# Optimization experiments

Measured on AMD Instinct MI355X. Metric: run time of the kernel, lower is better.

Reference implementation:

```python
import jax, jax.numpy as jnp
import numpy as np
from jax import lax

B, K, S = 1, 4, 1024
D = 1024          # hidden_size
DI = 2048         # intermediate_size = 2*D (expand=2)
N = 16            # ssm state size
DT_RANK = 64      # ceil(D/16)
CONV_K = 4
N_LAYERS = 48
CARD = 2048       # vocab
EPS = 1e-5


def setup_inputs() -> dict:
    key = jax.random.key(0)
    ks = jax.random.split(key, 10)
    sc = 0.02
    sequence = jax.random.randint(ks[0], (B, K, S), 0, CARD)
    emb_W = jax.random.normal(ks[1], (K, CARD, D), jnp.float32) * sc
    norm_w = jnp.ones((N_LAYERS, D), jnp.float32)
    in_W = jax.random.normal(ks[2], (N_LAYERS, 2 * DI, D), jnp.float32) * sc
    conv_w = jax.random.normal(ks[3], (N_LAYERS, DI, CONV_K), jnp.float32) * sc
    conv_b = jnp.zeros((N_LAYERS, DI), jnp.float32)
    x_W = jax.random.normal(ks[4], (N_LAYERS, DT_RANK + 2 * N, DI), jnp.float32) * sc
    dt_W = jax.random.normal(ks[5], (N_LAYERS, DI, DT_RANK), jnp.float32) * sc
    dt_b = jax.random.normal(ks[6], (N_LAYERS, DI), jnp.float32) * 0.1
    # HF Mamba init: A_log = log([1..N]) broadcast over channels
    A_log = jnp.log(jnp.broadcast_to(jnp.arange(1, N + 1, dtype=jnp.float32), (N_LAYERS, DI, N)))
    D_skip = jnp.ones((N_LAYERS, DI), jnp.float32)
    out_W = jax.random.normal(ks[7], (N_LAYERS, D, DI), jnp.float32) * sc
    normf_w = jnp.ones((D,), jnp.float32)
    head_W = jax.random.normal(ks[8], (K, CARD, D), jnp.float32) * sc
    head_b = jnp.zeros((K, CARD), jnp.float32)
    return {"sequence": sequence, "emb_W": emb_W, "norm_w": norm_w, "in_W": in_W,
            "conv_w": conv_w, "conv_b": conv_b, "x_W": x_W, "dt_W": dt_W, "dt_b": dt_b,
            "A_log": A_log, "D_skip": D_skip, "out_W": out_W, "normf_w": normf_w,
            "head_W": head_W, "head_b": head_b}


def rmsnorm(x, w):
    return x * lax.rsqrt(jnp.mean(x * x, -1, keepdims=True) + EPS) * w


def mamba_block(x, p):
    """One HF MambaBlock: residual + RMSNorm + MambaMixer (selective scan)."""
    norm_w, in_W, conv_w, conv_b, x_W, dt_W, dt_b, A_log, D_skip, out_W = p
    res = x
    h = rmsnorm(x, norm_w)
    proj = h @ in_W.T                                  # (B,S,2*DI)
    xz, gate = jnp.split(proj, 2, axis=-1)
    # causal depthwise conv1d, kernel 4
    xc = jnp.transpose(xz, (0, 2, 1))                  # (B,DI,S)
    xc = lax.conv_general_dilated(xc, conv_w[:, None, :], (1,), [(CONV_K - 1, 0)],
                                  feature_group_count=DI,
                                  dimension_numbers=("NCH", "OIH", "NCH"))
    xc = xc + conv_b[None, :, None]
    u = jax.nn.silu(jnp.transpose(xc, (0, 2, 1)))      # (B,S,DI)
    ssm_in = u @ x_W.T                                 # (B,S,DT_RANK+2N)
    dt_r, Bm, Cm = jnp.split(ssm_in, [DT_RANK, DT_RANK + N], axis=-1)
    dt = jax.nn.softplus(dt_r @ dt_W.T + dt_b)         # (B,S,DI)
    A = -jnp.exp(A_log)                                # (DI,N)

    def step(hst, inp):
        dt_t, B_t, C_t, u_t = inp                      # (B,DI),(B,N),(B,N),(B,DI)
        dA = jnp.exp(dt_t[:, :, None] * A)             # (B,DI,N)
        hst = dA * hst + (dt_t * u_t)[:, :, None] * B_t[:, None, :]
        y = jnp.einsum("bdn,bn->bd", hst, C_t)
        return hst, y

    h0 = jnp.zeros((B, DI, N), x.dtype)
    _, ys = lax.scan(step, h0, (dt.swapaxes(0, 1), Bm.swapaxes(0, 1),
                                Cm.swapaxes(0, 1), u.swapaxes(0, 1)))
    y = ys.swapaxes(0, 1) + u * D_skip                 # (B,S,DI)
    y = y * jax.nn.silu(gate)
    return res + y @ out_W.T


mamba_block_ckpt = jax.checkpoint(mamba_block)


def reference(sequence, emb_W, norm_w, in_W, conv_w, conv_b, x_W, dt_W, dt_b,
              A_log, D_skip, out_W, normf_w, head_W, head_b):
    # sum of K token-stream embeddings
    x = emb_W[jnp.arange(K)[None, :, None], sequence].sum(1)   # (B,S,D)

    def layer(x, p):
        return mamba_block_ckpt(x, p), None

    x, _ = lax.scan(layer, x, (norm_w, in_W, conv_w, conv_b, x_W, dt_W, dt_b,
                               A_log, D_skip, out_W))
    x = rmsnorm(x, normf_w)
    logits = jnp.einsum("bsd,kvd->bksv", x, head_W) + head_b[None, :, None, :]
    return logits                                              # (B,K,S,CARD)
```

## Files before the change

### kernel.cpp

```cpp
#include <hip/hip_runtime.h>
#include <hip/hip_bf16.h>

#define S 1024
#define D 1024
#define DI 2048
#define NSTATE 16
#define DTR 64
#define XPD 96
#define NL 48
#define CARD 2048
#define KTOK 4

typedef __attribute__((ext_vector_type(8))) short bf16x8;
typedef __attribute__((ext_vector_type(4))) float f32x4;
struct __align__(16) US8 { unsigned long long a, b; };

__device__ __forceinline__ unsigned short f2bf(float f) {
    unsigned u = __builtin_bit_cast(unsigned, f);
    return (unsigned short)((u + 0x7fffu + ((u >> 16) & 1u)) >> 16);
}
__device__ __forceinline__ float bf2f(unsigned short u) {
    return __builtin_bit_cast(float, (unsigned)u << 16);
}
__device__ __forceinline__ float fsilu(float x) { return x / (1.f + __expf(-x)); }
__device__ __forceinline__ float fsoftplus(float x) {
    return fmaxf(x, 0.f) + log1pf(__expf(-fabsf(x)));
}
template<int CTRL>
__device__ __forceinline__ float dpp_add(float v) {
    int m = __builtin_amdgcn_update_dpp(0, __builtin_bit_cast(int, v), CTRL, 0xF, 0xF, true);
    return v + __builtin_bit_cast(float, m);
}
__device__ __forceinline__ void gload_lds16(const void* g, void* l) {
    __builtin_amdgcn_global_load_lds((const __attribute__((address_space(1))) void*)g,
                                     (__attribute__((address_space(3))) void*)l, 16, 0, 0);
}
template<int N> __device__ __forceinline__ void wait_vm() {
    if constexpr (N == 0)      asm volatile("s_waitcnt vmcnt(0)" ::: "memory");
    else if constexpr (N == 3) asm volatile("s_waitcnt vmcnt(3)" ::: "memory");
    else if constexpr (N == 4) asm volatile("s_waitcnt vmcnt(4)" ::: "memory");
    else if constexpr (N == 6) asm volatile("s_waitcnt vmcnt(6)" ::: "memory");
    else                       asm volatile("s_waitcnt vmcnt(8)" ::: "memory");
}

__global__ __launch_bounds__(256) void cvt4_kernel(const float* __restrict__ a, long NA,
                                                   const float* __restrict__ b, long NB,
                                                   const float* __restrict__ c, long NC,
                                                   const float* __restrict__ d, long ND,
                                                   unsigned short* __restrict__ oa,
                                                   unsigned short* __restrict__ ob,
                                                   unsigned short* __restrict__ oc,
                                                   unsigned short* __restrict__ od) {
    long i = (long)blockIdx.x * 256 + threadIdx.x;
    const float* src; unsigned short* dst; long off;
    if (i < NA)                    { src = a; dst = oa; off = i; }
    else if (i < NA + NB)          { src = b; dst = ob; off = i - NA; }
    else if (i < NA + NB + NC)     { src = c; dst = oc; off = i - NA - NB; }
    else                            { src = d; dst = od; off = i - NA - NB - NC; }
    f32x4 v0 = *(const f32x4*)&src[off * 8];
    f32x4 v1 = *(const f32x4*)&src[off * 8 + 4];
    US8 pk;
    pk.a = (unsigned long long)f2bf(v0[0]) | ((unsigned long long)f2bf(v0[1]) << 16)
         | ((unsigned long long)f2bf(v0[2]) << 32) | ((unsigned long long)f2bf(v0[3]) << 48);
    pk.b = (unsigned long long)f2bf(v1[0]) | ((unsigned long long)f2bf(v1[1]) << 16)
         | ((unsigned long long)f2bf(v1[2]) << 32) | ((unsigned long long)f2bf(v1[3]) << 48);
    *(US8*)&dst[off * 8] = pk;
}

__global__ __launch_bounds__(256) void embed_kernel(const int* __restrict__ seq,
                                                    const float* __restrict__ embW,
                                                    float* __restrict__ x) {
    int s = blockIdx.x, t = threadIdx.x;
    f32x4 acc = (f32x4)0.f;
#pragma unroll
    for (int k = 0; k < KTOK; ++k) {
        int tok = seq[k * S + s];
        const f32x4 v = *(const f32x4*)&embW[((size_t)k * CARD + tok) * D + t * 4];
        acc += v;
    }
    *(f32x4*)&x[(size_t)s * D + t * 4] = acc;
}

__global__ __launch_bounds__(256) void rmsnorm_kernel(const float* __restrict__ x,
                                                      const float* __restrict__ w,
                                                      unsigned short* __restrict__ o) {
    int row = blockIdx.x, t = threadIdx.x;
    f32x4 v = *(const f32x4*)&x[(size_t)row * D + t * 4];
    float ss = v[0]*v[0] + v[1]*v[1] + v[2]*v[2] + v[3]*v[3];
#pragma unroll
    for (int off = 32; off >= 1; off >>= 1) ss += __shfl_xor(ss, off);
    __shared__ float red[4];
    int wave = t >> 6, lane = t & 63;
    if (lane == 0) red[wave] = ss;
    __syncthreads();
    ss = red[0] + red[1] + red[2] + red[3];
    float rs = rsqrtf(ss * (1.f / D) + 1e-5f);
    f32x4 wv = *(const f32x4*)&w[t * 4];
    unsigned long long pk = 0;
#pragma unroll
    for (int j = 0; j < 4; ++j)
        pk |= (unsigned long long)f2bf(v[j] * rs * wv[j]) << (16 * j);
    *(unsigned long long*)&o[(size_t)row * D + t * 4] = pk;
}

__global__ __launch_bounds__(256) void outred_rms_kernel(const float* __restrict__ part,
                                                         float* __restrict__ x,
                                                         const float* __restrict__ w,
                                                         unsigned short* __restrict__ o) {
    int row = blockIdx.x, t = threadIdx.x;
    size_t base = (size_t)row * D + t * 4;
    f32x4 v = *(const f32x4*)&x[base];
#pragma unroll
    for (int j = 0; j < 2; ++j)
        v += *(const f32x4*)&part[(size_t)j * (S * D) + base];
    *(f32x4*)&x[base] = v;
    float ss = v[0]*v[0] + v[1]*v[1] + v[2]*v[2] + v[3]*v[3];
#pragma unroll
    for (int off = 32; off >= 1; off >>= 1) ss += __shfl_xor(ss, off);
    __shared__ float red[4];
    int wave = t >> 6, lane = t & 63;
    if (lane == 0) red[wave] = ss;
    __syncthreads();
    ss = red[0] + red[1] + red[2] + red[3];
    float rs = rsqrtf(ss * (1.f / D) + 1e-5f);
    f32x4 wv = *(const f32x4*)&w[t * 4];
    unsigned long long pk = 0;
#pragma unroll
    for (int j = 0; j < 4; ++j)
        pk |= (unsigned long long)f2bf(v[j] * rs * wv[j]) << (16 * j);
    *(unsigned long long*)&o[base] = pk;
}

__global__ __launch_bounds__(256) void ssm_reduce_kernel(const float* __restrict__ part,
                                                         float* __restrict__ ssm,
                                                         unsigned short* __restrict__ ssmb) {
    int i = blockIdx.x * 256 + threadIdx.x;
    float a = 0.f;
#pragma unroll
    for (int j = 0; j < 8; ++j)
        a += part[(size_t)j * (S * XPD) + i];
    ssm[i] = a;
    ssmb[i] = f2bf(a);
}

__global__ __launch_bounds__(256) void conv_silu_kernel(const float* __restrict__ proj,
                                                        const float* __restrict__ cw,
                                                        const float* __restrict__ cb,
                                                        unsigned short* __restrict__ ub) {
    int idx = blockIdx.x * 256 + threadIdx.x;
    int s = idx >> 11, c = idx & (DI - 1);
    f32x4 w = *(const f32x4*)&cw[c * 4];
    float acc = cb[c];
#pragma unroll
    for (int t = 0; t < 4; ++t) {
        int ss = s - 3 + t;
        if (ss >= 0) acc = fmaf(w[t], proj[(size_t)ss * 4096 + c], acc);
    }
    ub[idx] = f2bf(acc * (1.f / (1.f + __expf(-acc))));
}

__global__ __launch_bounds__(1024, 2) void scan2_kernel(const unsigned short* __restrict__ ssmb,
                                                        const unsigned short* __restrict__ dtWb,
                                                        const float* __restrict__ dtb,
                                                        const unsigned short* __restrict__ ub,
                                                        const float* __restrict__ ssm,
                                                        const float* __restrict__ proj,
                                                        const float* __restrict__ A_log,
                                                        const float* __restrict__ Dsk,
                                                        unsigned short* __restrict__ yfb) {
    __shared__ float sdu[S * 4 * 2];
    __shared__ float sP[1024], sQ[1024];

    const int tid = threadIdx.x;
    const int d0 = blockIdx.x * 4;
    const int chunk = tid >> 6;
    const int lane = tid & 63;
    const int dl = (tid >> 4) & 3;
    const int n = tid & 15;
    const int sbase = chunk * 64;

#pragma unroll
    for (int i = 0; i < 4; ++i) {
        int idx = tid + i * 1024;
        int s = idx >> 2, d2 = idx & 3;
        sdu[idx * 2 + 1] = bf2f(ub[(size_t)s * DI + d0 + d2]);
    }

    {
        const int lr = lane & 15;
        const int lk = (lane >> 4) << 3;
        f32x4 dacc[4];
#pragma unroll
        for (int m = 0; m < 4; ++m) dacc[m] = (f32x4)0.f;
        bf16x8 wf0 = *(const bf16x8*)&dtWb[(size_t)(d0 + lr) * DTR + lk];
        bf16x8 wf1 = *(const bf16x8*)&dtWb[(size_t)(d0 + lr) * DTR + 32 + lk];
#pragma unroll
        for (int m = 0; m < 4; ++m) {
            const unsigned short* arow = &ssmb[(size_t)(sbase + m * 16 + lr) * XPD];
            bf16x8 a0 = *(const bf16x8*)&arow[lk];
            bf16x8 a1 = *(const bf16x8*)&arow[32 + lk];
            dacc[m] = __builtin_amdgcn_mfma_f32_16x16x32_bf16(a0, wf0, dacc[m], 0, 0, 0);
            dacc[m] = __builtin_amdgcn_mfma_f32_16x16x32_bf16(a1, wf1, dacc[m], 0, 0, 0);
        }
        if (lr < 4) {
            float bias = dtb[d0 + lr];
            const int rb = (lane >> 4) << 2;
#pragma unroll
            for (int m = 0; m < 4; ++m)
#pragma unroll
                for (int j = 0; j < 4; ++j) {
                    int sl = sbase + m * 16 + rb + j;
                    sdu[(sl * 4 + lr) * 2 + 0] = fsoftplus(dacc[m][j] + bias);
                }
        }
    }
    const float Av = -__expf(A_log[(d0 + dl) * NSTATE + n]);
    const float Dv = Dsk[d0 + dl];
    __syncthreads();

    float h = 0.f, P = 1.f;
#pragma unroll 4
    for (int i = 0; i < 64; ++i) {
        int s = sbase + i;
        float2 du = *(const float2*)&sdu[(s * 4 + dl) * 2];
        float Bs  = ssm[s * XPD + DTR + n];
        float dA  = __expf(du.x * Av);
        P *= dA;
        h = fmaf(dA, h, du.x * du.y * Bs);
    }
    const int pqb = (dl * 16 + n) * 16;
    sP[pqb + chunk] = P;
    sQ[pqb + chunk] = h;
    __syncthreads();
    float hi = 0.f;
    for (int j = 0; j < chunk; ++j) hi = fmaf(sP[pqb + j], hi, sQ[pqb + j]);
    h = hi;
#pragma unroll 2
    for (int i = 0; i < 64; ++i) {
        int s = sbase + i;
        float2 du = *(const float2*)&sdu[(s * 4 + dl) * 2];
        float Bs  = ssm[s * XPD + DTR + n];
        float Cs  = ssm[s * XPD + DTR + NSTATE + n];
        float dA  = __expf(du.x * Av);
        h = fmaf(dA, h, du.x * du.y * Bs);
        float pc = h * Cs;
        pc = dpp_add<0xB1>(pc);
        pc = dpp_add<0x4E>(pc);
        pc = dpp_add<0x124>(pc);
        pc = dpp_add<0x128>(pc);
        if (n == 0) {
            float g = proj[(size_t)s * 4096 + 2048 + d0 + dl];
            yfb[(size_t)s * DI + d0 + dl] = f2bf((pc + du.y * Dv) * fsilu(g));
        }
    }
}

template<int MR, int NR, int EPI, int KSPLIT, int ABF16, int DBUF>
__global__ __launch_bounds__(256) void gemm_bt(const void* __restrict__ Av, int lda,
                                               const unsigned short* __restrict__ W,
                                               float* __restrict__ C,
                                               int K, int N,
                                               const float* __restrict__ bias) {
    constexpr int BM = MR * 32;
    constexpr int BN = NR * 32;
    static_assert(DBUF == 0 || ((BM == 64 || BM == 128) && BN == 128 && ABF16 == 1), "dbuf shape");
    constexpr int NBUF = DBUF ? 3 : 1;
    __shared__ unsigned short As[NBUF][BM][32];
    __shared__ unsigned short Ws[NBUF][BN][32];
    const int tid = threadIdx.x;
    const int lane = tid & 63;
    const int wave = tid >> 6;
    const int wr = wave >> 1, wc = wave & 1;
    const int m0 = blockIdx.y * BM;
    const int n0 = blockIdx.x * BN;
    const unsigned short* Wp = W;
    const float* biasp = bias;
    float* Cp = C;
    if (EPI == 3) {
        size_t z = blockIdx.z;
        Wp += z * (size_t)N * K;
        Cp += z * (size_t)1024 * N;
        biasp += z * N;
    }
    if (EPI == 5)
        Cp = C + (size_t)blockIdx.z * 1024 * N;
    f32x4 acc[MR][NR];
#pragma unroll
    for (int m = 0; m < MR; ++m)
#pragma unroll
        for (int n = 0; n < NR; ++n) acc[m][n] = (f32x4)0.f;

    const int lr = lane & 15;
    const int lk = (lane >> 4) << 3;
    const int grow = lane >> 2;
    const int gcol = (lane & 3) << 3;

    const int kc = (KSPLIT > 1) ? blockIdx.z : 0;
    const int Kc = K / KSPLIT;
    const int kbeg = kc * Kc;

    if constexpr (DBUF) {
        const unsigned short* Ab = (const unsigned short*)Av;
        const int nt = Kc >> 5;
        constexpr int L = BM / 64 + 2;
        auto ISSUE = [&](int t, int buf) {
            const int k0 = kbeg + t * 32;
#pragma unroll
            for (int u2 = wave; u2 < BM / 16; u2 += 4)
                gload_lds16(&Ab[(size_t)(m0 + u2 * 16 + grow) * lda + k0 + gcol],
                            &As[buf][u2 * 16][0]);
#pragma unroll
            for (int u2 = wave; u2 < BN / 16; u2 += 4)
                gload_lds16(&Wp[(size_t)(n0 + u2 * 16 + grow) * K + k0 + gcol],
                            &Ws[buf][u2 * 16][0]);
        };
        ISSUE(0, 0);
        if (nt > 1) ISSUE(1, 1);
        int nb = 2;
        int cb = 0;
        for (int t = 0; t < nt; ++t) {
            if (t + 2 < nt) {
                ISSUE(t + 2, nb);
                if (++nb == 3) nb = 0;
            }
            const int rem = nt - 1 - t;
            if (rem >= 2)      wait_vm<2 * L>();
            else if (rem == 1) wait_vm<L>();
            else               wait_vm<0>();
            __builtin_amdgcn_s_barrier();
            bf16x8 af[MR], wf[NR];
#pragma unroll
            for (int m = 0; m < MR; ++m)
                af[m] = *(const bf16x8*)&As[cb][wr * (MR * 16) + m * 16 + lr][lk];
#pragma unroll
            for (int n = 0; n < NR; ++n)
                wf[n] = *(const bf16x8*)&Ws[cb][wc * (NR * 16) + n * 16 + lr][lk];
            asm volatile("s_waitcnt lgkmcnt(0)" ::: "memory");
            __builtin_amdgcn_s_barrier();
            if (++cb == 3) cb = 0;
#pragma unroll
            for (int m = 0; m < MR; ++m)
#pragma unroll
                for (int n = 0; n < NR; ++n)
                    acc[m][n] = __builtin_amdgcn_mfma_f32_16x16x32_bf16(af[m], wf[n], acc[m][n], 0, 0, 0);
        }
    } else {
        for (int k0 = kbeg; k0 < kbeg + Kc; k0 += 32) {
            __syncthreads();
            if (ABF16) {
                const unsigned short* Ab = (const unsigned short*)Av;
#pragma unroll
                for (int u2 = wave; u2 < BM / 16; u2 += 4)
                    gload_lds16(&Ab[(size_t)(m0 + u2 * 16 + grow) * lda + k0 + gcol],
                                &As[0][u2 * 16][0]);
            } else {
                const float* Af = (const float*)Av;
#pragma unroll
                for (int i = 0; i < BM / 32; ++i) {
                    int idx = tid + i * 256;
                    int row = idx >> 3, c4 = (idx & 7) << 2;
                    f32x4 v = *(const f32x4*)&Af[(size_t)(m0 + row) * lda + k0 + c4];
                    unsigned long long pk = (unsigned long long)f2bf(v[0])
                                          | ((unsigned long long)f2bf(v[1]) << 16)
                                          | ((unsigned long long)f2bf(v[2]) << 32)
                                          | ((unsigned long long)f2bf(v[3]) << 48);
                    *(unsigned long long*)&As[0][row][c4] = pk;
                }
            }
#pragma unroll
            for (int u2 = wave; u2 < BN / 16; u2 += 4)
                gload_lds16(&Wp[(size_t)(n0 + u2 * 16 + grow) * K + k0 + gcol],
                            &Ws[0][u2 * 16][0]);
            __syncthreads();
            bf16x8 af[MR], wf[NR];
#pragma unroll
            for (int m = 0; m < MR; ++m)
                af[m] = *(const bf16x8*)&As[0][wr * (MR * 16) + m * 16 + lr][lk];
#pragma unroll
            for (int n = 0; n < NR; ++n)
                wf[n] = *(const bf16x8*)&Ws[0][wc * (NR * 16) + n * 16 + lr][lk];
#pragma unroll
            for (int m = 0; m < MR; ++m)
#pragma unroll
                for (int n = 0; n < NR; ++n)
                    acc[m][n] = __builtin_amdgcn_mfma_f32_16x16x32_bf16(af[m], wf[n], acc[m][n], 0, 0, 0);
        }
    }

    const int mo = m0 + wr * (MR * 16);
    const int no = n0 + wc * (NR * 16);
    const int rbase = (lane >> 4) << 2;
#pragma unroll
    for (int m = 0; m < MR; ++m) {
#pragma unroll
        for (int n = 0; n < NR; ++n) {
            int col = no + n * 16 + lr;
#pragma unroll
            for (int j = 0; j < 4; ++j) {
                int row = mo + m * 16 + rbase + j;
                float v = acc[m][n][j];
                if (EPI == 1) v = fsoftplus(v + biasp[col]);
                else if (EPI == 3) v += biasp[col];
                Cp[(size_t)row * N + col] = v;
            }
        }
    }
}

#define IN_E   ((size_t)4096 * 1024)
#define OUT_E  ((size_t)1024 * 2048)
#define X_E    ((size_t)XPD * 2048)
#define DT_E   ((size_t)2048 * 64)
#define HEAD_E ((size_t)KTOK * CARD * 1024)

extern "C" void kernel_launch(void* const* d_in, const int* in_sizes, int n_in,
                              void* d_out, int out_size, void* d_ws, size_t ws_size,
                              hipStream_t stream) {
    const int*   seq     = (const int*)d_in[0];
    const float* embW    = (const float*)d_in[1];
    const float* norm_w  = (const float*)d_in[2];
    const float* in_W    = (const float*)d_in[3];
    const float* conv_w  = (const float*)d_in[4];
    const float* conv_b  = (const float*)d_in[5];
    const float* x_W     = (const float*)d_in[6];
    const float* dt_W    = (const float*)d_in[7];
    const float* dt_b    = (const float*)d_in[8];
    const float* A_log   = (const float*)d_in[9];
    const float* D_skip  = (const float*)d_in[10];
    const float* out_W   = (const float*)d_in[11];
    const float* normf_w = (const float*)d_in[12];
    const float* head_W  = (const float*)d_in[13];
    const float* head_b  = (const float*)d_in[14];

    float* ws   = (float*)d_ws;
    float* x    = ws;
    float* proj = x    + (size_t)S * D;
    float* ssm  = proj + (size_t)S * 4096;
    float* xpart = ssm + (size_t)S * 128;
    unsigned short* hnb  = (unsigned short*)(xpart + (size_t)S * DI);
    unsigned short* ub   = hnb  + (size_t)S * D;
    unsigned short* yfb  = ub   + (size_t)S * DI;
    unsigned short* ssmb = yfb  + (size_t)S * DI;
    unsigned short* wbase = ssmb + (size_t)S * 128;
    float* opart = proj;

    size_t actBytes = (char*)wbase - (char*)ws;
    size_t perLayerE = IN_E + OUT_E + X_E + DT_E;
    bool bulk = ws_size >= actBytes + (48 * perLayerE + HEAD_E) * 2 + 256;

    unsigned short* inWb, *outWb, *xWb, *dtWb, *headWb;
    size_t strIn, strOut, strX, strDt;
    if (bulk) {
        inWb  = wbase;
        outWb = inWb  + 48 * IN_E;
        xWb   = outWb + 48 * OUT_E;
        dtWb  = xWb   + 48 * X_E;
        headWb = dtWb + 48 * DT_E;
        strIn = IN_E; strOut = OUT_E; strX = X_E; strDt = DT_E;
    } else {
        inWb  = wbase;
        outWb = inWb  + IN_E;
        xWb   = outWb + OUT_E;
        dtWb  = xWb   + X_E;
        headWb = dtWb + DT_E;
        strIn = strOut = strX = strDt = 0;
    }

    embed_kernel<<<S, 256, 0, stream>>>(seq, embW, x);
    rmsnorm_kernel<<<S, 256, 0, stream>>>(x, norm_w, hnb);
    cvt4_kernel<<<(unsigned)(HEAD_E / 8 / 256), 256, 0, stream>>>(
        head_W, (long)(HEAD_E / 8), nullptr, 0, nullptr, 0, nullptr, 0,
        headWb, nullptr, nullptr, nullptr);
    if (bulk) {
        long na = (long)(48 * IN_E / 8), nb = (long)(48 * OUT_E / 8);
        long nc = (long)(48 * X_E / 8),  nd = (long)(48 * DT_E / 8);
        cvt4_kernel<<<(unsigned)((na + nb + nc + nd) / 256), 256, 0, stream>>>(
            in_W, na, out_W, nb, x_W, nc, dt_W, nd, inWb, outWb, xWb, dtWb);
    }

    for (int l = 0; l < NL; ++l) {
        if (!bulk) {
            cvt4_kernel<<<(unsigned)(perLayerE / 8 / 256), 256, 0, stream>>>(
                in_W + (size_t)l * IN_E, (long)(IN_E / 8),
                out_W + (size_t)l * OUT_E, (long)(OUT_E / 8),
                x_W + (size_t)l * X_E, (long)(X_E / 8),
                dt_W + (size_t)l * DT_E, (long)(DT_E / 8),
                inWb, outWb, xWb, dtWb);
        }
        gemm_bt<2, 4, 0, 1, 1, 1><<<dim3(32, 16), 256, 0, stream>>>(hnb, D,
            inWb + (size_t)l * strIn, proj, D, 4096, nullptr);
        conv_silu_kernel<<<(S * DI) / 256, 256, 0, stream>>>(proj,
            conv_w + (size_t)l * DI * 4, conv_b + (size_t)l * DI, ub);
        gemm_bt<2, 3, 5, 8, 1, 0><<<dim3(1, 16, 8), 256, 0, stream>>>(ub, DI,
            xWb + (size_t)l * strX, xpart, DI, XPD, nullptr);
        ssm_reduce_kernel<<<(S * XPD) / 256, 256, 0, stream>>>(xpart, ssm, ssmb);
        scan2_kernel<<<DI / 4, 1024, 0, stream>>>(ssmb, dtWb + (size_t)l * strDt,
            dt_b + (size_t)l * DI, ub, ssm, proj,
            A_log + (size_t)l * DI * NSTATE, D_skip + (size_t)l * DI, yfb);
        gemm_bt<2, 4, 5, 2, 1, 1><<<dim3(8, 16, 2), 256, 0, stream>>>(yfb, DI,
            outWb + (size_t)l * strOut, opart, DI, D, nullptr);
        outred_rms_kernel<<<S, 256, 0, stream>>>(opart, x,
            (l + 1 < NL) ? (norm_w + (size_t)(l + 1) * D) : normf_w, hnb);
    }

    gemm_bt<4, 4, 3, 1, 1, 1><<<dim3(16, 8, 4), 256, 0, stream>>>(hnb, D, headWb,
        (float*)d_out, D, CARD, head_b);
}
```

Measured before the change: 7.394 ms.

## Fuse causal conv+SiLU into x-projection GEMM A-load and vectorize scan output gating

Removes the standalone conv_silu kernel by computing the depthwise causal conv and SiLU while loading the A tile of the x_proj GEMM, which also writes the bf16 u activations for the scan. The scan kernel now stages y in shared memory and applies the SiLU gate with vectorized loads and packed bf16 stores instead of scattered per-element writes. This saves one launch and a round trip through memory, at the cost of each GEMM tile re-reading four proj rows and doing the conv math inline, with the x_proj GEMM's A-load now on a non-async fp32 path.

```diff
diff --git a/kernel.cpp b/kernel.cpp
--- a/kernel.cpp
+++ b/kernel.cpp
@@ -143,22 +143,6 @@
     ssmb[i] = f2bf(a);
 }
 
-__global__ __launch_bounds__(256) void conv_silu_kernel(const float* __restrict__ proj,
-                                                        const float* __restrict__ cw,
-                                                        const float* __restrict__ cb,
-                                                        unsigned short* __restrict__ ub) {
-    int idx = blockIdx.x * 256 + threadIdx.x;
-    int s = idx >> 11, c = idx & (DI - 1);
-    f32x4 w = *(const f32x4*)&cw[c * 4];
-    float acc = cb[c];
-#pragma unroll
-    for (int t = 0; t < 4; ++t) {
-        int ss = s - 3 + t;
-        if (ss >= 0) acc = fmaf(w[t], proj[(size_t)ss * 4096 + c], acc);
-    }
-    ub[idx] = f2bf(acc * (1.f / (1.f + __expf(-acc))));
-}
-
 __global__ __launch_bounds__(1024, 2) void scan2_kernel(const unsigned short* __restrict__ ssmb,
                                                         const unsigned short* __restrict__ dtWb,
                                                         const float* __restrict__ dtb,
@@ -170,6 +154,7 @@
                                                         unsigned short* __restrict__ yfb) {
     __shared__ float sdu[S * 4 * 2];
     __shared__ float sP[1024], sQ[1024];
+    __shared__ float sy[S * 4];
 
     const int tid = threadIdx.x;
     const int d0 = blockIdx.x * 4;
@@ -248,19 +233,31 @@
         pc = dpp_add<0x4E>(pc);
         pc = dpp_add<0x124>(pc);
         pc = dpp_add<0x128>(pc);
-        if (n == 0) {
-            float g = proj[(size_t)s * 4096 + 2048 + d0 + dl];
-            yfb[(size_t)s * DI + d0 + dl] = f2bf((pc + du.y * Dv) * fsilu(g));
-        }
-    }
-}
-
-template<int MR, int NR, int EPI, int KSPLIT, int ABF16, int DBUF>
+        if (n == 0)
+            sy[s * 4 + dl] = pc + du.y * Dv;
+    }
+    __syncthreads();
+    {
+        int s = tid;
+        f32x4 yv = *(const f32x4*)&sy[s * 4];
+        f32x4 g  = *(const f32x4*)&proj[(size_t)s * 4096 + 2048 + d0];
+        unsigned long long pk = 0;
+#pragma unroll
+        for (int j = 0; j < 4; ++j)
+            pk |= (unsigned long long)f2bf(yv[j] * fsilu(g[j])) << (16 * j);
+        *(unsigned long long*)&yfb[(size_t)s * DI + d0] = pk;
+    }
+}
+
+template<int MR, int NR, int EPI, int KSPLIT, int ABF16, int DBUF, int ACONV = 0>
 __global__ __launch_bounds__(256) void gemm_bt(const void* __restrict__ Av, int lda,
                                                const unsigned short* __restrict__ W,
                                                float* __restrict__ C,
                                                int K, int N,
-                                               const float* __restrict__ bias) {
+                                               const float* __restrict__ bias,
+                                               const float* __restrict__ cw,
+                                               const float* __restrict__ cb,
+                                               unsigned short* __restrict__ uout) {
     constexpr int BM = MR * 32;
     constexpr int BN = NR * 32;
     static_assert(DBUF == 0 || ((BM == 64 || BM == 128) && BN == 128 && ABF16 == 1), "dbuf shape");
@@ -317,7 +314,7 @@
         ISSUE(0, 0);
         if (nt > 1) ISSUE(1, 1);
         int nb = 2;
-        int cb = 0;
+        int cb2 = 0;
         for (int t = 0; t < nt; ++t) {
             if (t + 2 < nt) {
                 ISSUE(t + 2, nb);
@@ -331,13 +328,13 @@
             bf16x8 af[MR], wf[NR];
 #pragma unroll
             for (int m = 0; m < MR; ++m)
-                af[m] = *(const bf16x8*)&As[cb][wr * (MR * 16) + m * 16 + lr][lk];
+                af[m] = *(const bf16x8*)&As[cb2][wr * (MR * 16) + m * 16 + lr][lk];
 #pragma unroll
             for (int n = 0; n < NR; ++n)
-                wf[n] = *(const bf16x8*)&Ws[cb][wc * (NR * 16) + n * 16 + lr][lk];
+                wf[n] = *(const bf16x8*)&Ws[cb2][wc * (NR * 16) + n * 16 + lr][lk];
             asm volatile("s_waitcnt lgkmcnt(0)" ::: "memory");
             __builtin_amdgcn_s_barrier();
-            if (++cb == 3) cb = 0;
+            if (++cb2 == 3) cb2 = 0;
 #pragma unroll
             for (int m = 0; m < MR; ++m)
 #pragma unroll
@@ -347,7 +344,39 @@
     } else {
         for (int k0 = kbeg; k0 < kbeg + Kc; k0 += 32) {
             __syncthreads();
-            if (ABF16) {
+            if constexpr (ACONV) {
+                const float* Af = (const float*)Av;
+#pragma unroll
+                for (int i = 0; i < BM / 32; ++i) {
+                    int idx = tid + i * 256;
+                    int row = idx >> 3, c4 = (idx & 7) << 2;
+                    int s = m0 + row, c = k0 + c4;
+                    f32x4 a = *(const f32x4*)&cb[c];
+                    f32x4 w0 = *(const f32x4*)&cw[(c + 0) * 4];
+                    f32x4 w1 = *(const f32x4*)&cw[(c + 1) * 4];
+                    f32x4 w2 = *(const f32x4*)&cw[(c + 2) * 4];
+                    f32x4 w3 = *(const f32x4*)&cw[(c + 3) * 4];
+#pragma unroll
+                    for (int t = 0; t < 4; ++t) {
+                        int ss = s - 3 + t;
+                        if (ss >= 0) {
+                            f32x4 tv = *(const f32x4*)&Af[(size_t)ss * lda + c];
+                            a[0] = fmaf(w0[t], tv[0], a[0]);
+                            a[1] = fmaf(w1[t], tv[1], a[1]);
+                            a[2] = fmaf(w2[t], tv[2], a[2]);
+                            a[3] = fmaf(w3[t], tv[3], a[3]);
+                        }
+                    }
+                    unsigned long long pk = 0;
+#pragma unroll
+                    for (int j = 0; j < 4; ++j) {
+                        float r = a[j] * (1.f / (1.f + __expf(-a[j])));
+                        pk |= (unsigned long long)f2bf(r) << (16 * j);
+                    }
+                    *(unsigned long long*)&As[0][row][c4] = pk;
+                    *(unsigned long long*)&uout[(size_t)s * DI + c] = pk;
+                }
+            } else if (ABF16) {
                 const unsigned short* Ab = (const unsigned short*)Av;
 #pragma unroll
                 for (int u2 = wave; u2 < BM / 16; u2 += 4)
@@ -488,21 +517,20 @@
                 inWb, outWb, xWb, dtWb);
         }
         gemm_bt<2, 4, 0, 1, 1, 1><<<dim3(32, 16), 256, 0, stream>>>(hnb, D,
-            inWb + (size_t)l * strIn, proj, D, 4096, nullptr);
-        conv_silu_kernel<<<(S * DI) / 256, 256, 0, stream>>>(proj,
+            inWb + (size_t)l * strIn, proj, D, 4096, nullptr, nullptr, nullptr, nullptr);
+        gemm_bt<2, 3, 5, 8, 0, 0, 1><<<dim3(1, 16, 8), 256, 0, stream>>>(proj, 4096,
+            xWb + (size_t)l * strX, xpart, DI, XPD, nullptr,
             conv_w + (size_t)l * DI * 4, conv_b + (size_t)l * DI, ub);
-        gemm_bt<2, 3, 5, 8, 1, 0><<<dim3(1, 16, 8), 256, 0, stream>>>(ub, DI,
-            xWb + (size_t)l * strX, xpart, DI, XPD, nullptr);
         ssm_reduce_kernel<<<(S * XPD) / 256, 256, 0, stream>>>(xpart, ssm, ssmb);
         scan2_kernel<<<DI / 4, 1024, 0, stream>>>(ssmb, dtWb + (size_t)l * strDt,
             dt_b + (size_t)l * DI, ub, ssm, proj,
             A_log + (size_t)l * DI * NSTATE, D_skip + (size_t)l * DI, yfb);
         gemm_bt<2, 4, 5, 2, 1, 1><<<dim3(8, 16, 2), 256, 0, stream>>>(yfb, DI,
-            outWb + (size_t)l * strOut, opart, DI, D, nullptr);
+            outWb + (size_t)l * strOut, opart, DI, D, nullptr, nullptr, nullptr, nullptr);
         outred_rms_kernel<<<S, 256, 0, stream>>>(opart, x,
             (l + 1 < NL) ? (norm_w + (size_t)(l + 1) * D) : normf_w, hnb);
     }
 
     gemm_bt<4, 4, 3, 1, 1, 1><<<dim3(16, 8, 4), 256, 0, stream>>>(hnb, D, headWb,
-        (float*)d_out, D, CARD, head_b);
-}
+        (float*)d_out, D, CARD, head_b, nullptr, nullptr, nullptr);
+}
```

Result: no change. 7.337 ms (-0.8%).
